# Performance work log

Measured on AMD Instinct MI355X. Metric: run time of the kernel, lower is better.

## Reference

```python
import jax, jax.numpy as jnp
import numpy as np

N = 50000
IN_CH = 128
HEADS = 4
OUT_CH = 32
E = 800000
NEG_SLOPE = 0.2


def setup_inputs() -> dict:
    key = jax.random.key(0)
    k1, k2, k3, k4, k5, k6 = jax.random.split(key, 6)
    x = jax.random.normal(k1, (N, IN_CH), dtype=jnp.float32)
    edge_index = jax.random.randint(k2, (2, E), 0, N, dtype=jnp.int64)
    # learned params (PyG GATv2Conv: lin_l, lin_r weights, att vector, bias)
    s = 1.0 / np.sqrt(IN_CH)
    W_l = jax.random.uniform(k3, (IN_CH, HEADS, OUT_CH), jnp.float32, -s, s)
    W_r = jax.random.uniform(k4, (IN_CH, HEADS, OUT_CH), jnp.float32, -s, s)
    att = jax.random.uniform(k5, (HEADS, OUT_CH), jnp.float32, -s, s)
    bias = jax.random.uniform(k6, (HEADS * OUT_CH,), jnp.float32, -s, s)
    return {"x": x, "edge_index": edge_index, "W_l": W_l, "W_r": W_r,
            "att": att, "bias": bias}


def reference(x, edge_index, W_l, W_r, att, bias):
    # add self loops (PyG default add_self_loops=True)
    loops = jnp.arange(N, dtype=edge_index.dtype)
    src = jnp.concatenate([edge_index[0], loops])  # message source j
    dst = jnp.concatenate([edge_index[1], loops])  # message target i

    # node projections: [N, H, C]
    x_l = jnp.einsum('nd,dhc->nhc', x, W_l)  # source-side
    x_r = jnp.einsum('nd,dhc->nhc', x, W_r)  # target-side

    # GATv2 attention logits per edge: a^T LeakyReLU(x_l[j] + x_r[i])
    e = jax.nn.leaky_relu(x_l[src] + x_r[dst], NEG_SLOPE)  # [Etot, H, C]
    score = jnp.einsum('ehc,hc->eh', e, att)               # [Etot, H]

    # segment softmax over incoming edges of each destination node
    m = jax.ops.segment_max(score, dst, num_segments=N)    # [N, H]
    m = jnp.where(jnp.isfinite(m), m, 0.0)
    ex = jnp.exp(score - m[dst])                           # [Etot, H]
    denom = jax.ops.segment_sum(ex, dst, num_segments=N)   # [N, H]
    alpha = ex / denom[dst]                                # [Etot, H]

    # scatter-aggregate weighted messages
    msg = alpha[:, :, None] * x_l[src]                     # [Etot, H, C]
    out = jax.ops.segment_sum(msg, dst, num_segments=N)    # [N, H, C]

    # concat heads + bias
    return out.reshape(N, HEADS * OUT_CH) + bias
```

## Files before the change

kernel.cpp:

```cpp
#include <hip/hip_runtime.h>
#include <math.h>

#define N_NODES 50000
#define IN_CH   128
#define TOT_CH  128
#define NEDGE   800000
#define ETOT    (NEDGE + N_NODES)
#define MTILES  ((N_NODES + 63) / 64)
#define NBUCK   ((N_NODES + 255) / 256)
#define BCAP    8192
#define EPB     4096
#define NBIN    ((ETOT + EPB - 1) / EPB)

#define OFF_XL      ((size_t)0)
#define OFF_EBUF    ((size_t)12800000)
#define OFF_XR      ((size_t)25600000)
#define OFF_SRC     ((size_t)38400000)
#define OFF_BT      ((size_t)44900352)
#define OFF_GCUR    ((size_t)45000064)
#define OFF_ROWPTR  ((size_t)51200000)

typedef float f32x4 __attribute__((ext_vector_type(4)));
typedef short s16x8 __attribute__((ext_vector_type(8)));

__device__ __forceinline__ unsigned f2bf(float f) {
    unsigned u = __float_as_uint(f);
    return (u + 0x7fffu + ((u >> 16) & 1u)) >> 16;
}
__device__ __forceinline__ float bflo(unsigned u) { return __uint_as_float(u << 16); }
__device__ __forceinline__ float bfhi(unsigned u) { return __uint_as_float(u & 0xffff0000u); }

__device__ __forceinline__ int SWZ(int row, int byteoff) {
    return row * 256 + (byteoff ^ ((row & 7) << 4));
}

__global__ __launch_bounds__(256) void zero_kernel(int* __restrict__ gcur) {
    if (threadIdx.x < NBUCK) gcur[threadIdx.x] = 0;
}

__global__ __launch_bounds__(256) void k1_kernel(
    const float* __restrict__ Wl, const float* __restrict__ Wr,
    unsigned* __restrict__ btg, const int* __restrict__ ei,
    int* __restrict__ gcur, unsigned* __restrict__ ebuf)
{
    __shared__ int lcnt[256];
    __shared__ int lbase[256];
    const int bid = blockIdx.x;
    const int tid = threadIdx.x;

    if (bid < NBIN) {
        lcnt[tid] = 0;
        __syncthreads();
        const int base = bid * EPB;
        int sv[16], dv[16];
#pragma unroll
        for (int u = 0; u < 16; ++u) {
            const int e = base + u * 256 + tid;
            int s32 = 0, d32 = -1;
            if (e < ETOT) {
                if (e < NEDGE) { s32 = ei[e]; d32 = ei[NEDGE + e]; }
                else           { s32 = d32 = e - NEDGE; }
                atomicAdd(&lcnt[d32 >> 8], 1);
            }
            sv[u] = s32; dv[u] = d32;
        }
        __syncthreads();
        if (tid < NBUCK) {
            const int v = lcnt[tid];
            lbase[tid] = v ? atomicAdd(&gcur[tid], v) : 0;
        }
        __syncthreads();
        lcnt[tid] = 0;
        __syncthreads();
#pragma unroll
        for (int u = 0; u < 16; ++u) {
            const int d32 = dv[u];
            if (d32 >= 0) {
                const int b = d32 >> 8;
                const int p = lbase[b] + atomicAdd(&lcnt[b], 1);
                ebuf[b * BCAP + p] = (unsigned)sv[u] | ((unsigned)(d32 & 255) << 16);
            }
        }
    } else {
        const int g = (bid - NBIN) * 256 + tid;
        if (g < 256 * 64) {
            const int n = g >> 6, kk = g & 63;
            const float* W = (n < 128) ? Wl : Wr;
            const int nc = n & 127;
            const float a = W[(size_t)(2 * kk) * 128 + nc];
            const float b = W[(size_t)(2 * kk + 1) * 128 + nc];
            btg[g] = f2bf(a) | (f2bf(b) << 16);
        }
    }
}

__global__ __launch_bounds__(256) void k2_kernel(
    const float* __restrict__ x, const unsigned* __restrict__ btg,
    unsigned* __restrict__ xl_bf, unsigned* __restrict__ xr_bf,
    const unsigned* __restrict__ ebuf, const int* __restrict__ gcur,
    int2* __restrict__ rowptr2, int* __restrict__ ssrc)
{
    __shared__ __align__(16) unsigned char smem[32768];
    __shared__ int wsum[4];
    const int bid = blockIdx.x;
    const int tid = threadIdx.x;

    if (bid < NBUCK) {
        int* lcnt = (int*)smem;
        int* lcur = ((int*)smem) + 256;
        const int ecnt  = gcur[bid];
        const int ebase = bid * BCAP;
        lcnt[tid] = 0;
        __syncthreads();
        for (int k = tid; k < ecnt; k += 256)
            atomicAdd(&lcnt[(ebuf[ebase + k] >> 16) & 255], 1);
        __syncthreads();
        const int lane = tid & 63, wid = tid >> 6;
        const int v = lcnt[tid];
        int s = v;
#pragma unroll
        for (int off = 1; off < 64; off <<= 1) {
            int t = __shfl_up(s, off);
            if (lane >= off) s += t;
        }
        if (lane == 63) wsum[wid] = s;
        __syncthreads();
        if (tid == 0) {
            int acc = 0;
#pragma unroll
            for (int w = 0; w < 4; ++w) { int t = wsum[w]; wsum[w] = acc; acc += t; }
        }
        __syncthreads();
        const int gpos = ebase + wsum[wid] + s - v;
        const int node = (bid << 8) + tid;
        if (node < N_NODES) rowptr2[node] = make_int2(gpos, gpos + v);
        lcur[tid] = gpos;
        __syncthreads();
        for (int k = tid; k < ecnt; k += 256) {
            const unsigned ed = ebuf[ebase + k];
            const int p = atomicAdd(&lcur[(ed >> 16) & 255], 1);
            ssrc[p] = (int)(ed & 0xffffu);
        }
        return;
    }

    unsigned char* Al = smem;
    unsigned char* Bl = smem + 16384;
    const int mt = bid - NBUCK;
    const int mbase = mt * 64;
    const int l  = tid & 63;
    const int wv = tid >> 6;

    {
        const int r = tid >> 2, q = tid & 3;
        int gm = mbase + r;
        gm = (gm < N_NODES) ? gm : (N_NODES - 1);
        const float* xrow = x + (size_t)gm * IN_CH + q * 32;
#pragma unroll
        for (int i = 0; i < 8; ++i) {
            const float4 xv = *(const float4*)(xrow + i * 4);
            uint2 p;
            p.x = f2bf(xv.x) | (f2bf(xv.y) << 16);
            p.y = f2bf(xv.z) | (f2bf(xv.w) << 16);
            *(uint2*)(Al + SWZ(r, q * 64 + i * 8)) = p;
        }
    }
    {
        const int r = tid >> 2, q = tid & 3;
        const unsigned* brow = btg + (size_t)r * 64 + q * 16;
#pragma unroll
        for (int i = 0; i < 4; ++i) {
            const uint4 v = *(const uint4*)(brow + i * 4);
            *(uint4*)(Bl + SWZ(r, q * 64 + i * 16)) = v;
        }
    }
    __syncthreads();

    s16x8 af[4];
#pragma unroll
    for (int ks = 0; ks < 4; ++ks)
        af[ks] = *(const s16x8*)(Al + SWZ(wv * 16 + (l & 15), ks * 64 + (l >> 4) * 16));

    for (int nt4 = 0; nt4 < 4; ++nt4) {
        f32x4 acc[4];
#pragma unroll
        for (int n = 0; n < 4; ++n) acc[n] = (f32x4){0.f, 0.f, 0.f, 0.f};
#pragma unroll
        for (int nsub = 0; nsub < 4; ++nsub) {
#pragma unroll
            for (int ks = 0; ks < 4; ++ks) {
                const s16x8 bfr = *(const s16x8*)(Bl + SWZ(nsub * 16 + (l & 15), ks * 64 + (l >> 4) * 16));
                acc[nsub] = __builtin_amdgcn_mfma_f32_16x16x32_bf16(af[ks], bfr, acc[nsub], 0, 0, 0);
            }
        }
        unsigned* dstbuf = (nt4 < 2) ? xl_bf : xr_bf;
        const int ncol0 = (nt4 & 1) * 64;
#pragma unroll
        for (int nsub = 0; nsub < 4; ++nsub) {
            const int n = ncol0 + nsub * 16 + (l & 15);
#pragma unroll
            for (int reg = 0; reg < 4; ++reg) {
                const float v  = acc[nsub][reg];
                const float vp = __shfl_xor(v, 1);
                const int row = mbase + wv * 16 + (l >> 4) * 4 + reg;
                if (((l & 1) == 0) && row < N_NODES)
                    dstbuf[(size_t)row * 64 + (n >> 1)] = f2bf(v) | (f2bf(vp) << 16);
            }
        }
        if (nt4 == 3) break;
        __syncthreads();
        {
            const int r = tid >> 2, q = tid & 3;
            const unsigned* brow = btg + (size_t)((nt4 + 1) * 64 + r) * 64 + q * 16;
#pragma unroll
            for (int i = 0; i < 4; ++i) {
                const uint4 v = *(const uint4*)(brow + i * 4);
                *(uint4*)(Bl + SWZ(r, q * 64 + i * 16)) = v;
            }
        }
        __syncthreads();
    }
}

#define DPP_ADD(s, ctrl) do { \
        int _t = __builtin_amdgcn_update_dpp(0, __float_as_int(s), ctrl, 0xf, 0xf, true); \
        s += __int_as_float(_t); } while(0)

__global__ __launch_bounds__(256) void gat_kernel(
    const unsigned* __restrict__ xl_bf, const unsigned* __restrict__ xr_bf,
    const int2* __restrict__ rowptr2, const int* __restrict__ srcs,
    const float* __restrict__ att, const float* __restrict__ bias,
    float* __restrict__ out)
{
    const int l  = threadIdx.x & 63;
    const int wv = threadIdx.x >> 6;
    const int sl = l & 15;
    const int q  = l >> 4;
    const int i  = blockIdx.x * 16 + wv * 4 + q;
    const int c8 = sl * 8;
    const float LOG2E = 1.4426950408889634f;
    const float K23 = 0.66666669f;

    float a6[8], xr8[8];
    {
        const float4 A = *(const float4*)(att + c8);
        const float4 B = *(const float4*)(att + c8 + 4);
        a6[0] = 0.6f * LOG2E * A.x; a6[1] = 0.6f * LOG2E * A.y;
        a6[2] = 0.6f * LOG2E * A.z; a6[3] = 0.6f * LOG2E * A.w;
        a6[4] = 0.6f * LOG2E * B.x; a6[5] = 0.6f * LOG2E * B.y;
        a6[6] = 0.6f * LOG2E * B.z; a6[7] = 0.6f * LOG2E * B.w;
    }
    {
        const uint4 urv = *(const uint4*)(xr_bf + (size_t)i * 64 + sl * 4);
        xr8[0] = bflo(urv.x); xr8[1] = bfhi(urv.x);
        xr8[2] = bflo(urv.y); xr8[3] = bfhi(urv.y);
        xr8[4] = bflo(urv.z); xr8[5] = bfhi(urv.z);
        xr8[6] = bflo(urv.w); xr8[7] = bfhi(urv.w);
    }
    const int2 kr = rowptr2[i];
    int k = kr.x;
    const int kend = kr.y;

    float den = 0.f, b[8];
#pragma unroll
    for (int c = 0; c < 8; ++c) b[c] = 0.f;

    uint4 u;
    {
        const int jv = srcs[k];
        u = *(const uint4*)(xl_bf + (size_t)jv * 64 + sl * 4);
    }
    for (; k < kend; ++k) {
        const uint4 ucur = u;
        {
            const int kn = (k + 1 < kend) ? (k + 1) : k;
            const int jn = srcs[kn];
            u = *(const uint4*)(xl_bf + (size_t)jn * 64 + sl * 4);
        }
        float t[8];
        t[0] = bflo(ucur.x) + xr8[0]; t[1] = bfhi(ucur.x) + xr8[1];
        t[2] = bflo(ucur.y) + xr8[2]; t[3] = bfhi(ucur.y) + xr8[3];
        t[4] = bflo(ucur.z) + xr8[4]; t[5] = bfhi(ucur.z) + xr8[5];
        t[6] = bflo(ucur.w) + xr8[6]; t[7] = bfhi(ucur.w) + xr8[7];
        float s = 0.f;
#pragma unroll
        for (int c = 0; c < 8; ++c) {
            const float h = fmaf(K23, fabsf(t[c]), t[c]);
            s = fmaf(a6[c], h, s);
        }
        DPP_ADD(s, 0xB1);
        DPP_ADD(s, 0x4E);
        const float p = __builtin_amdgcn_exp2f(s);
        den += p;
#pragma unroll
        for (int c = 0; c < 8; ++c) b[c] = fmaf(p, t[c], b[c]);
    }

    const float inv = 1.f / den;
    const float4 bbA = *(const float4*)(bias + c8);
    const float4 bbB = *(const float4*)(bias + c8 + 4);
    float4 o1, o2;
    o1.x = fmaf(b[0], inv, bbA.x - xr8[0]);
    o1.y = fmaf(b[1], inv, bbA.y - xr8[1]);
    o1.z = fmaf(b[2], inv, bbA.z - xr8[2]);
    o1.w = fmaf(b[3], inv, bbA.w - xr8[3]);
    o2.x = fmaf(b[4], inv, bbB.x - xr8[4]);
    o2.y = fmaf(b[5], inv, bbB.y - xr8[5]);
    o2.z = fmaf(b[6], inv, bbB.z - xr8[6]);
    o2.w = fmaf(b[7], inv, bbB.w - xr8[7]);
    *(float4*)(out + (size_t)i * TOT_CH + c8)     = o1;
    *(float4*)(out + (size_t)i * TOT_CH + c8 + 4) = o2;
}

extern "C" void kernel_launch(void* const* d_in, const int* in_sizes, int n_in,
                              void* d_out, int out_size, void* d_ws, size_t ws_size,
                              hipStream_t stream) {
    const float* x    = (const float*)d_in[0];
    const int*   ei   = (const int*)d_in[1];
    const float* Wl   = (const float*)d_in[2];
    const float* Wr   = (const float*)d_in[3];
    const float* att  = (const float*)d_in[4];
    const float* bias = (const float*)d_in[5];
    float* out = (float*)d_out;
    char*  ws  = (char*)d_ws;

    unsigned* xl_bf = (unsigned*)(ws + OFF_XL);
    unsigned* ebuf  = (unsigned*)(ws + OFF_EBUF);
    unsigned* xr_bf = (unsigned*)(ws + OFF_XR);
    int*      ssrc  = (int*)(ws + OFF_SRC);
    unsigned* btg   = (unsigned*)(ws + OFF_BT);
    int*      gcur  = (int*)(ws + OFF_GCUR);
    int2*   rowptr2 = (int2*)(ws + OFF_ROWPTR);

    hipLaunchKernelGGL(zero_kernel, dim3(1), dim3(256), 0, stream, gcur);
    hipLaunchKernelGGL(k1_kernel, dim3(NBIN + 64), dim3(256), 0, stream,
                       Wl, Wr, btg, ei, gcur, ebuf);
    hipLaunchKernelGGL(k2_kernel, dim3(NBUCK + MTILES), dim3(256), 0, stream,
                       x, btg, xl_bf, xr_bf, ebuf, gcur, rowptr2, ssrc);
    hipLaunchKernelGGL(gat_kernel, dim3(N_NODES / 16), dim3(256), 0, stream,
                       xl_bf, xr_bf, rowptr2, ssrc, att, bias, out);
}
```

Baseline: 83.45 us.

## Regroup pipeline stages so GEMM overlaps edge binning and bucket placement runs alone

```diff
diff --git a/kernel.cpp b/kernel.cpp
--- a/kernel.cpp
+++ b/kernel.cpp
@@ -34,24 +34,41 @@
     return row * 256 + (byteoff ^ ((row & 7) << 4));
 }
 
-__global__ __launch_bounds__(256) void zero_kernel(int* __restrict__ gcur) {
-    if (threadIdx.x < NBUCK) gcur[threadIdx.x] = 0;
-}
-
-__global__ __launch_bounds__(256) void k1_kernel(
+__global__ __launch_bounds__(256) void ka_kernel(
     const float* __restrict__ Wl, const float* __restrict__ Wr,
-    unsigned* __restrict__ btg, const int* __restrict__ ei,
-    int* __restrict__ gcur, unsigned* __restrict__ ebuf)
+    unsigned* __restrict__ btg, int* __restrict__ gcur)
 {
-    __shared__ int lcnt[256];
-    __shared__ int lbase[256];
     const int bid = blockIdx.x;
     const int tid = threadIdx.x;
-
-    if (bid < NBIN) {
+    if (bid == 64) {
+        if (tid < NBUCK) gcur[tid] = 0;
+        return;
+    }
+    const int g = bid * 256 + tid;
+    const int n = g >> 6, kk = g & 63;
+    const float* W = (n < 128) ? Wl : Wr;
+    const int nc = n & 127;
+    const float a = W[(size_t)(2 * kk) * 128 + nc];
+    const float b = W[(size_t)(2 * kk + 1) * 128 + nc];
+    btg[g] = f2bf(a) | (f2bf(b) << 16);
+}
+
+__global__ __launch_bounds__(256) void kb_kernel(
+    const float* __restrict__ x, const unsigned* __restrict__ btg,
+    unsigned* __restrict__ xl_bf, unsigned* __restrict__ xr_bf,
+    const int* __restrict__ ei, int* __restrict__ gcur, unsigned* __restrict__ ebuf)
+{
+    __shared__ __align__(16) unsigned char smem[32768];
+    const int bid = blockIdx.x;
+    const int tid = threadIdx.x;
+
+    if (bid >= MTILES) {
+        int* lcnt  = (int*)smem;
+        int* lbase = ((int*)smem) + 256;
+        const int bin = bid - MTILES;
         lcnt[tid] = 0;
         __syncthreads();
-        const int base = bid * EPB;
+        const int base = bin * EPB;
         int sv[16], dv[16];
 #pragma unroll
         for (int u = 0; u < 16; ++u) {
@@ -81,72 +98,12 @@
                 ebuf[b * BCAP + p] = (unsigned)sv[u] | ((unsigned)(d32 & 255) << 16);
             }
         }
-    } else {
-        const int g = (bid - NBIN) * 256 + tid;
-        if (g < 256 * 64) {
-            const int n = g >> 6, kk = g & 63;
-            const float* W = (n < 128) ? Wl : Wr;
-            const int nc = n & 127;
-            const float a = W[(size_t)(2 * kk) * 128 + nc];
-            const float b = W[(size_t)(2 * kk + 1) * 128 + nc];
-            btg[g] = f2bf(a) | (f2bf(b) << 16);
-        }
-    }
-}
-
-__global__ __launch_bounds__(256) void k2_kernel(
-    const float* __restrict__ x, const unsigned* __restrict__ btg,
-    unsigned* __restrict__ xl_bf, unsigned* __restrict__ xr_bf,
-    const unsigned* __restrict__ ebuf, const int* __restrict__ gcur,
-    int2* __restrict__ rowptr2, int* __restrict__ ssrc)
-{
-    __shared__ __align__(16) unsigned char smem[32768];
-    __shared__ int wsum[4];
-    const int bid = blockIdx.x;
-    const int tid = threadIdx.x;
-
-    if (bid < NBUCK) {
-        int* lcnt = (int*)smem;
-        int* lcur = ((int*)smem) + 256;
-        const int ecnt  = gcur[bid];
-        const int ebase = bid * BCAP;
-        lcnt[tid] = 0;
-        __syncthreads();
-        for (int k = tid; k < ecnt; k += 256)
-            atomicAdd(&lcnt[(ebuf[ebase + k] >> 16) & 255], 1);
-        __syncthreads();
-        const int lane = tid & 63, wid = tid >> 6;
-        const int v = lcnt[tid];
-        int s = v;
-#pragma unroll
-        for (int off = 1; off < 64; off <<= 1) {
-            int t = __shfl_up(s, off);
-            if (lane >= off) s += t;
-        }
-        if (lane == 63) wsum[wid] = s;
-        __syncthreads();
-        if (tid == 0) {
-            int acc = 0;
-#pragma unroll
-            for (int w = 0; w < 4; ++w) { int t = wsum[w]; wsum[w] = acc; acc += t; }
-        }
-        __syncthreads();
-        const int gpos = ebase + wsum[wid] + s - v;
-        const int node = (bid << 8) + tid;
-        if (node < N_NODES) rowptr2[node] = make_int2(gpos, gpos + v);
-        lcur[tid] = gpos;
-        __syncthreads();
-        for (int k = tid; k < ecnt; k += 256) {
-            const unsigned ed = ebuf[ebase + k];
-            const int p = atomicAdd(&lcur[(ed >> 16) & 255], 1);
-            ssrc[p] = (int)(ed & 0xffffu);
-        }
         return;
     }
 
     unsigned char* Al = smem;
     unsigned char* Bl = smem + 16384;
-    const int mt = bid - NBUCK;
+    const int mt = bid;
     const int mbase = mt * 64;
     const int l  = tid & 63;
     const int wv = tid >> 6;
@@ -219,6 +176,49 @@
             }
         }
         __syncthreads();
+    }
+}
+
+__global__ __launch_bounds__(256) void place_kernel(
+    const unsigned* __restrict__ ebuf, const int* __restrict__ gcur,
+    int2* __restrict__ rowptr2, int* __restrict__ ssrc)
+{
+    __shared__ int lcnt[256];
+    __shared__ int lcur[256];
+    __shared__ int wsum[4];
+    const int b = blockIdx.x;
+    const int ecnt  = gcur[b];
+    const int ebase = b * BCAP;
+    const int tid = threadIdx.x, lane = tid & 63, wid = tid >> 6;
+    lcnt[tid] = 0;
+    __syncthreads();
+    for (int k = tid; k < ecnt; k += 256)
+        atomicAdd(&lcnt[(ebuf[ebase + k] >> 16) & 255], 1);
+    __syncthreads();
+    const int v = lcnt[tid];
+    int s = v;
+#pragma unroll
+    for (int off = 1; off < 64; off <<= 1) {
+        int t = __shfl_up(s, off);
+        if (lane >= off) s += t;
+    }
+    if (lane == 63) wsum[wid] = s;
+    __syncthreads();
+    if (tid == 0) {
+        int acc = 0;
+#pragma unroll
+        for (int w = 0; w < 4; ++w) { int t = wsum[w]; wsum[w] = acc; acc += t; }
+    }
+    __syncthreads();
+    const int gpos = ebase + wsum[wid] + s - v;
+    const int node = (b << 8) + tid;
+    if (node < N_NODES) rowptr2[node] = make_int2(gpos, gpos + v);
+    lcur[tid] = gpos;
+    __syncthreads();
+    for (int k = tid; k < ecnt; k += 256) {
+        const unsigned ed = ebuf[ebase + k];
+        const int p = atomicAdd(&lcur[(ed >> 16) & 255], 1);
+        ssrc[p] = (int)(ed & 0xffffu);
     }
 }
 
@@ -332,11 +332,11 @@
     int*      gcur  = (int*)(ws + OFF_GCUR);
     int2*   rowptr2 = (int2*)(ws + OFF_ROWPTR);
 
-    hipLaunchKernelGGL(zero_kernel, dim3(1), dim3(256), 0, stream, gcur);
-    hipLaunchKernelGGL(k1_kernel, dim3(NBIN + 64), dim3(256), 0, stream,
-                       Wl, Wr, btg, ei, gcur, ebuf);
-    hipLaunchKernelGGL(k2_kernel, dim3(NBUCK + MTILES), dim3(256), 0, stream,
-                       x, btg, xl_bf, xr_bf, ebuf, gcur, rowptr2, ssrc);
+    hipLaunchKernelGGL(ka_kernel, dim3(65), dim3(256), 0, stream, Wl, Wr, btg, gcur);
+    hipLaunchKernelGGL(kb_kernel, dim3(MTILES + NBIN), dim3(256), 0, stream,
+                       x, btg, xl_bf, xr_bf, ei, gcur, ebuf);
+    hipLaunchKernelGGL(place_kernel, dim3(NBUCK), dim3(256), 0, stream,
+                       ebuf, gcur, rowptr2, ssrc);
     hipLaunchKernelGGL(gat_kernel, dim3(N_NODES / 16), dim3(256), 0, stream,
                        xl_bf, xr_bf, rowptr2, ssrc, att, bias, out);
 }
```

New measurement: 83.91 us. Within noise of the previous version (+0.5%).

## Read projection weights directly from global memory in the MFMA projection and merge the zeroing kernel

Applied to the files above, without the earlier changes.

```diff
diff --git a/kernel.cpp b/kernel.cpp
--- a/kernel.cpp
+++ b/kernel.cpp
@@ -34,62 +34,62 @@
     return row * 256 + (byteoff ^ ((row & 7) << 4));
 }
 
-__global__ __launch_bounds__(256) void zero_kernel(int* __restrict__ gcur) {
-    if (threadIdx.x < NBUCK) gcur[threadIdx.x] = 0;
-}
-
-__global__ __launch_bounds__(256) void k1_kernel(
+__global__ __launch_bounds__(256) void ka_kernel(
     const float* __restrict__ Wl, const float* __restrict__ Wr,
-    unsigned* __restrict__ btg, const int* __restrict__ ei,
-    int* __restrict__ gcur, unsigned* __restrict__ ebuf)
+    unsigned* __restrict__ btg, int* __restrict__ gcur)
+{
+    const int bid = blockIdx.x;
+    const int tid = threadIdx.x;
+    if (bid == 64) {
+        if (tid < NBUCK) gcur[tid] = 0;
+        return;
+    }
+    const int g = bid * 256 + tid;
+    const int n = g >> 6, kk = g & 63;
+    const float* W = (n < 128) ? Wl : Wr;
+    const int nc = n & 127;
+    const float a = W[(size_t)(2 * kk) * 128 + nc];
+    const float b = W[(size_t)(2 * kk + 1) * 128 + nc];
+    btg[g] = f2bf(a) | (f2bf(b) << 16);
+}
+
+__global__ __launch_bounds__(256) void binscatter_kernel(
+    const int* __restrict__ ei, int* __restrict__ gcur, unsigned* __restrict__ ebuf)
 {
     __shared__ int lcnt[256];
     __shared__ int lbase[256];
     const int bid = blockIdx.x;
     const int tid = threadIdx.x;
-
-    if (bid < NBIN) {
-        lcnt[tid] = 0;
-        __syncthreads();
-        const int base = bid * EPB;
-        int sv[16], dv[16];
-#pragma unroll
-        for (int u = 0; u < 16; ++u) {
-            const int e = base + u * 256 + tid;
-            int s32 = 0, d32 = -1;
-            if (e < ETOT) {
-                if (e < NEDGE) { s32 = ei[e]; d32 = ei[NEDGE + e]; }
-                else           { s32 = d32 = e - NEDGE; }
-                atomicAdd(&lcnt[d32 >> 8], 1);
-            }
-            sv[u] = s32; dv[u] = d32;
-        }
-        __syncthreads();
-        if (tid < NBUCK) {
-            const int v = lcnt[tid];
-            lbase[tid] = v ? atomicAdd(&gcur[tid], v) : 0;
-        }
-        __syncthreads();
-        lcnt[tid] = 0;
-        __syncthreads();
-#pragma unroll
-        for (int u = 0; u < 16; ++u) {
-            const int d32 = dv[u];
-            if (d32 >= 0) {
-                const int b = d32 >> 8;
-                const int p = lbase[b] + atomicAdd(&lcnt[b], 1);
-                ebuf[b * BCAP + p] = (unsigned)sv[u] | ((unsigned)(d32 & 255) << 16);
-            }
-        }
-    } else {
-        const int g = (bid - NBIN) * 256 + tid;
-        if (g < 256 * 64) {
-            const int n = g >> 6, kk = g & 63;
-            const float* W = (n < 128) ? Wl : Wr;
-            const int nc = n & 127;
-            const float a = W[(size_t)(2 * kk) * 128 + nc];
-            const float b = W[(size_t)(2 * kk + 1) * 128 + nc];
-            btg[g] = f2bf(a) | (f2bf(b) << 16);
+    lcnt[tid] = 0;
+    __syncthreads();
+    const int base = bid * EPB;
+    int sv[16], dv[16];
+#pragma unroll
+    for (int u = 0; u < 16; ++u) {
+        const int e = base + u * 256 + tid;
+        int s32 = 0, d32 = -1;
+        if (e < ETOT) {
+            if (e < NEDGE) { s32 = ei[e]; d32 = ei[NEDGE + e]; }
+            else           { s32 = d32 = e - NEDGE; }
+            atomicAdd(&lcnt[d32 >> 8], 1);
+        }
+        sv[u] = s32; dv[u] = d32;
+    }
+    __syncthreads();
+    if (tid < NBUCK) {
+        const int v = lcnt[tid];
+        lbase[tid] = v ? atomicAdd(&gcur[tid], v) : 0;
+    }
+    __syncthreads();
+    lcnt[tid] = 0;
+    __syncthreads();
+#pragma unroll
+    for (int u = 0; u < 16; ++u) {
+        const int d32 = dv[u];
+        if (d32 >= 0) {
+            const int b = d32 >> 8;
+            const int p = lbase[b] + atomicAdd(&lcnt[b], 1);
+            ebuf[b * BCAP + p] = (unsigned)sv[u] | ((unsigned)(d32 & 255) << 16);
         }
     }
 }
@@ -100,7 +100,7 @@
     const unsigned* __restrict__ ebuf, const int* __restrict__ gcur,
     int2* __restrict__ rowptr2, int* __restrict__ ssrc)
 {
-    __shared__ __align__(16) unsigned char smem[32768];
+    __shared__ __align__(16) unsigned char smem[16384];
     __shared__ int wsum[4];
     const int bid = blockIdx.x;
     const int tid = threadIdx.x;
@@ -145,7 +145,6 @@
     }
 
     unsigned char* Al = smem;
-    unsigned char* Bl = smem + 16384;
     const int mt = bid - NBUCK;
     const int mbase = mt * 64;
     const int l  = tid & 63;
@@ -165,15 +164,6 @@
             *(uint2*)(Al + SWZ(r, q * 64 + i * 8)) = p;
         }
     }
-    {
-        const int r = tid >> 2, q = tid & 3;
-        const unsigned* brow = btg + (size_t)r * 64 + q * 16;
-#pragma unroll
-        for (int i = 0; i < 4; ++i) {
-            const uint4 v = *(const uint4*)(brow + i * 4);
-            *(uint4*)(Bl + SWZ(r, q * 64 + i * 16)) = v;
-        }
-    }
     __syncthreads();
 
     s16x8 af[4];
@@ -181,15 +171,17 @@
     for (int ks = 0; ks < 4; ++ks)
         af[ks] = *(const s16x8*)(Al + SWZ(wv * 16 + (l & 15), ks * 64 + (l >> 4) * 16));
 
+#pragma unroll
     for (int nt4 = 0; nt4 < 4; ++nt4) {
         f32x4 acc[4];
 #pragma unroll
         for (int n = 0; n < 4; ++n) acc[n] = (f32x4){0.f, 0.f, 0.f, 0.f};
 #pragma unroll
         for (int nsub = 0; nsub < 4; ++nsub) {
+            const unsigned* bcol = btg + (size_t)(nt4 * 64 + nsub * 16 + (l & 15)) * 64 + (l >> 4) * 4;
 #pragma unroll
             for (int ks = 0; ks < 4; ++ks) {
-                const s16x8 bfr = *(const s16x8*)(Bl + SWZ(nsub * 16 + (l & 15), ks * 64 + (l >> 4) * 16));
+                const s16x8 bfr = *(const s16x8*)(bcol + ks * 16);
                 acc[nsub] = __builtin_amdgcn_mfma_f32_16x16x32_bf16(af[ks], bfr, acc[nsub], 0, 0, 0);
             }
         }
@@ -207,18 +199,6 @@
                     dstbuf[(size_t)row * 64 + (n >> 1)] = f2bf(v) | (f2bf(vp) << 16);
             }
         }
-        if (nt4 == 3) break;
-        __syncthreads();
-        {
-            const int r = tid >> 2, q = tid & 3;
-            const unsigned* brow = btg + (size_t)((nt4 + 1) * 64 + r) * 64 + q * 16;
-#pragma unroll
-            for (int i = 0; i < 4; ++i) {
-                const uint4 v = *(const uint4*)(brow + i * 4);
-                *(uint4*)(Bl + SWZ(r, q * 64 + i * 16)) = v;
-            }
-        }
-        __syncthreads();
     }
 }
 
@@ -332,9 +312,8 @@
     int*      gcur  = (int*)(ws + OFF_GCUR);
     int2*   rowptr2 = (int2*)(ws + OFF_ROWPTR);
 
-    hipLaunchKernelGGL(zero_kernel, dim3(1), dim3(256), 0, stream, gcur);
-    hipLaunchKernelGGL(k1_kernel, dim3(NBIN + 64), dim3(256), 0, stream,
-                       Wl, Wr, btg, ei, gcur, ebuf);
+    hipLaunchKernelGGL(ka_kernel, dim3(65), dim3(256), 0, stream, Wl, Wr, btg, gcur);
+    hipLaunchKernelGGL(binscatter_kernel, dim3(NBIN), dim3(256), 0, stream, ei, gcur, ebuf);
     hipLaunchKernelGGL(k2_kernel, dim3(NBUCK + MTILES), dim3(256), 0, stream,
                        x, btg, xl_bf, xr_bf, ebuf, gcur, rowptr2, ssrc);
     hipLaunchKernelGGL(gat_kernel, dim3(N_NODES / 16), dim3(256), 0, stream,
```

After: 102.5 us. +22.9%, slower.
